# Performance work log

Measured on AMD Instinct MI355X. Metric: run time of the kernel, lower is better.

Reference implementation:

```python
import jax, jax.numpy as jnp
import numpy as np

B = 4096
E = 1024   # input_size (embedding)
H = 1024   # hidden_size
C = 1024   # context_vector_size
D = E + H + C  # combined_vector_size


def setup_inputs() -> dict:
    key = jax.random.key(0)
    ks = jax.random.split(key, 20)
    s_gate = 1.0 / np.sqrt(D)
    s_c = 1.0 / np.sqrt(C)
    s_h = 1.0 / np.sqrt(H)
    s_e = 1.0 / np.sqrt(E)
    return {
        "previous_embedded_caption": jax.random.normal(ks[0], (B, E), jnp.float32),
        "previous_hidden_state": jax.random.normal(ks[1], (B, H), jnp.float32),
        "previous_cell_state": jax.random.normal(ks[2], (B, H), jnp.float32),
        "current_context_vector": jax.random.normal(ks[3], (B, C), jnp.float32),
        "Wi": jax.random.uniform(ks[4], (H, D), jnp.float32, -s_gate, s_gate),
        "bi": jax.random.uniform(ks[5], (H,), jnp.float32, -s_gate, s_gate),
        "Wf": jax.random.uniform(ks[6], (H, D), jnp.float32, -s_gate, s_gate),
        "bf": jax.random.uniform(ks[7], (H,), jnp.float32, -s_gate, s_gate),
        "Wo": jax.random.uniform(ks[8], (H, D), jnp.float32, -s_gate, s_gate),
        "bo": jax.random.uniform(ks[9], (H,), jnp.float32, -s_gate, s_gate),
        "Wg": jax.random.uniform(ks[10], (H, D), jnp.float32, -s_gate, s_gate),
        "bg": jax.random.uniform(ks[11], (H,), jnp.float32, -s_gate, s_gate),
        "Wc": jax.random.uniform(ks[12], (E, C), jnp.float32, -s_c, s_c),
        "bc": jax.random.uniform(ks[13], (E,), jnp.float32, -s_c, s_c),
        "Wh": jax.random.uniform(ks[14], (E, H), jnp.float32, -s_h, s_h),
        "bh": jax.random.uniform(ks[15], (E,), jnp.float32, -s_h, s_h),
        "Wp": jax.random.uniform(ks[16], (E, E), jnp.float32, -s_e, s_e),
        "bp": jax.random.uniform(ks[17], (E,), jnp.float32, -s_e, s_e),
    }


def reference(previous_embedded_caption, previous_hidden_state, previous_cell_state,
              current_context_vector, Wi, bi, Wf, bf, Wo, bo, Wg, bg,
              Wc, bc, Wh, bh, Wp, bp):
    # combined vector [B, D]
    combined = jnp.concatenate(
        [previous_embedded_caption, previous_hidden_state, current_context_vector], axis=1)
    i = jax.nn.sigmoid(combined @ Wi.T + bi)
    f = jax.nn.sigmoid(combined @ Wf.T + bf)
    o = jax.nn.sigmoid(combined @ Wo.T + bo)
    g = jnp.tanh(combined @ Wg.T + bg)
    cell = f * previous_cell_state + i * g           # [B, H]
    hidden = o * jnp.tanh(cell)                      # [B, H]
    resid = previous_embedded_caption + (hidden @ Wh.T + bh) + (current_context_vector @ Wc.T + bc)
    prediction = resid @ Wp.T + bp                   # [B, E]
    return (prediction, hidden, cell)
```

## Files before the change

### kernel.cpp

```cpp
#include <hip/hip_runtime.h>
#include <stdint.h>

#define BATCH 4096
#define EHC   1024
#define DCOMB 3072
#define NTOT  ((size_t)BATCH * EHC)
#define WGATE ((size_t)EHC * DCOMB)
#define WSML  ((size_t)EHC * EHC)

#define BM 128
#define BK 64

typedef __bf16 bf16x8 __attribute__((ext_vector_type(8)));
typedef float  f32x4  __attribute__((ext_vector_type(4)));

__device__ inline unsigned short f2b(float f) {
    unsigned int x = __float_as_uint(f);
    unsigned int r = (x + 0x7fffu + ((x >> 16) & 1u)) >> 16;
    return (unsigned short)r;
}
__device__ inline float sigmoid_f(float x) { return 1.0f / (1.0f + __expf(-x)); }
__device__ inline float tanh_f(float x) {
    float xa = fminf(fmaxf(x, -15.0f), 15.0f);
    float e = __expf(2.0f * xa);
    return (e - 1.0f) / (e + 1.0f);
}

__device__ inline void load16(const void* g, void* l) {
    __builtin_amdgcn_global_load_lds(
        (const __attribute__((address_space(1))) void*)g,
        (__attribute__((address_space(3))) void*)l, 16, 0, 0);
}

__global__ __launch_bounds__(256)
void cvt_all(const float* __restrict__ s0, const float* __restrict__ s1,
             const float* __restrict__ s2, const float* __restrict__ s3,
             const float* __restrict__ s4, const float* __restrict__ s5,
             const float* __restrict__ s6, const float* __restrict__ s7,
             const float* __restrict__ s8, const float* __restrict__ s9,
             short* __restrict__ dst)
{
    const unsigned b = blockIdx.x;
    const float* src = s0; unsigned st = 0;
    if (b >= 2048)  { src = s1; st = 2048;  }
    if (b >= 4096)  { src = s2; st = 4096;  }
    if (b >= 6144)  { src = s3; st = 6144;  }
    if (b >= 7680)  { src = s4; st = 7680;  }
    if (b >= 9216)  { src = s5; st = 9216;  }
    if (b >= 10752) { src = s6; st = 10752; }
    if (b >= 12288) { src = s7; st = 12288; }
    if (b >= 12800) { src = s8; st = 12800; }
    if (b >= 13312) { src = s9; st = 13312; }
    size_t soff = ((size_t)(b - st) * 2048) + (size_t)threadIdx.x * 8;
    size_t doff = ((size_t)b * 2048) + (size_t)threadIdx.x * 8;
    float4 a = *(const float4*)(src + soff);
    float4 c = *(const float4*)(src + soff + 4);
    uint4 v;
    v.x = (unsigned)f2b(a.x) | ((unsigned)f2b(a.y) << 16);
    v.y = (unsigned)f2b(a.z) | ((unsigned)f2b(a.w) << 16);
    v.z = (unsigned)f2b(c.x) | ((unsigned)f2b(c.y) << 16);
    v.w = (unsigned)f2b(c.z) | ((unsigned)f2b(c.w) << 16);
    *(uint4*)(dst + doff) = v;
}

template <int MODE>
__global__ __launch_bounds__(256, 2)
void gemm_fused(const short* __restrict__ A0, const short* __restrict__ A1,
                const short* __restrict__ A2,
                const short* __restrict__ W0, const short* __restrict__ W1,
                const short* __restrict__ W2, const short* __restrict__ W3,
                const float* __restrict__ b0, const float* __restrict__ b1,
                const float* __restrict__ b2, const float* __restrict__ b3,
                const float* __restrict__ extra,
                void* __restrict__ outv)
{
    constexpr int BNT = (MODE == 1) ? 128 : 64;
    constexpr int NI  = BNT / 32;
    constexpr int WNW = BNT / 2;

    const int nblk = blockIdx.x;
    const int mblk = blockIdx.y;
    const int tid  = threadIdx.x;
    const int lane = tid & 63;
    const int wave = tid >> 6;
    const int wm = wave >> 1;
    const int wn = wave & 1;
    const int l15 = lane & 15;
    const int l4  = lane >> 4;

    __shared__ short As[BM * BK];
    __shared__ short Bs[BNT * BK];

    const int K = (MODE == 1) ? DCOMB : (MODE == 2 ? 2048 : 1024);
    const int wstride = (MODE == 1) ? DCOMB : 1024;

    int gate = 0;
    const short* Wsel = W0;
    const float* bsel = b0;
    if (MODE == 1) {
        gate = nblk >> 3;
        Wsel = (gate == 0) ? W0 : (gate == 1) ? W1 : (gate == 2) ? W2 : W3;
        bsel = (gate == 0) ? b0 : (gate == 1) ? b1 : (gate == 2) ? b2 : b3;
    }
    const int wrowbase = ((MODE == 1) ? (nblk & 7) : nblk) * BNT;

    int aoff[4], woff[NI];
#pragma unroll
    for (int j = 0; j < 4; j++) {
        int c  = j * 256 + tid;
        int r  = c >> 3;
        int qg = (c & 7) ^ (r & 7);
        aoff[j] = (mblk * BM + r) * 1024 + qg * 8;
    }
#pragma unroll
    for (int j = 0; j < NI; j++) {
        int c  = j * 256 + tid;
        int r  = c >> 3;
        int qg = (c & 7) ^ (r & 7);
        woff[j] = (wrowbase + r) * wstride + qg * 8;
    }

    int a_ld[2][4], b_ld[2][NI];
#pragma unroll
    for (int s = 0; s < 2; s++) {
#pragma unroll
        for (int i = 0; i < 4; i++) {
            int q = s * 4 + l4;
            int rowA = wm * 64 + i * 16 + l15;
            a_ld[s][i] = (rowA * 8 + (q ^ (rowA & 7))) * 8;
        }
#pragma unroll
        for (int i = 0; i < NI; i++) {
            int q = s * 4 + l4;
            int rowB = wn * WNW + i * 16 + l15;
            b_ld[s][i] = (rowB * 8 + (q ^ (rowB & 7))) * 8;
        }
    }

    f32x4 acc[4][NI];
#pragma unroll
    for (int i = 0; i < 4; i++)
#pragma unroll
        for (int j = 0; j < NI; j++) acc[i][j] = (f32x4){0.f, 0.f, 0.f, 0.f};

    const int KT = K / BK;
    for (int kt = 0; kt < KT; ++kt) {
        const int k0   = kt * BK;
        const int seg  = (MODE == 3) ? 0 : (k0 >> 10);
        const int acol = k0 & 1023;
        const int wcol = (MODE == 1) ? k0 : acol;
        const short* Aseg = (seg == 0) ? A0 : (seg == 1) ? A1 : A2;
        const short* Wt   = (MODE == 1) ? Wsel : ((seg == 0) ? W0 : W1);

        __syncthreads();
#pragma unroll
        for (int j = 0; j < 4; j++)
            load16(Aseg + aoff[j] + acol, &As[(j * 256 + tid) * 8]);
#pragma unroll
        for (int j = 0; j < NI; j++)
            load16(Wt + woff[j] + wcol, &Bs[(j * 256 + tid) * 8]);
        __syncthreads();

#pragma unroll
        for (int s = 0; s < 2; s++) {
            bf16x8 af[4], bv[NI];
#pragma unroll
            for (int i = 0; i < 4; i++) af[i] = *(const bf16x8*)(As + a_ld[s][i]);
#pragma unroll
            for (int i = 0; i < NI; i++) bv[i] = *(const bf16x8*)(Bs + b_ld[s][i]);
#pragma unroll
            for (int mi = 0; mi < 4; mi++)
#pragma unroll
                for (int ni = 0; ni < NI; ni++)
                    acc[mi][ni] = __builtin_amdgcn_mfma_f32_16x16x32_bf16(
                        af[mi], bv[ni], acc[mi][ni], 0, 0, 0);
        }
    }

#pragma unroll
    for (int ni = 0; ni < NI; ni++) {
        const int col = nblk * BNT + wn * WNW + ni * 16 + l15;
        float bias_v;
        if (MODE == 1)      bias_v = bsel[col & 1023];
        else if (MODE == 2) bias_v = b0[col] + b1[col];
        else                bias_v = b0[col];
#pragma unroll
        for (int mi = 0; mi < 4; mi++) {
#pragma unroll
            for (int r = 0; r < 4; r++) {
                const int row = mblk * BM + wm * 64 + mi * 16 + l4 * 4 + r;
                float v = acc[mi][ni][r] + bias_v;
                if (MODE == 1) {
                    v = fminf(fmaxf(v, -30.0f), 30.0f);
                    v = (gate < 3) ? sigmoid_f(v) : tanh_f(v);
                    ((short*)outv)[(size_t)gate * NTOT + (size_t)row * 1024 + (col & 1023)]
                        = (short)f2b(v);
                } else if (MODE == 2) {
                    v += extra[(size_t)row * 1024 + col];
                    ((short*)outv)[(size_t)row * 1024 + col] = (short)f2b(v);
                } else {
                    ((float*)outv)[(size_t)row * 1024 + col] = v;
                }
            }
        }
    }
}

__global__ __launch_bounds__(256)
void lstm_cell(const short* __restrict__ gates, const float* __restrict__ pc,
               float* __restrict__ hid_f, float* __restrict__ cell_f,
               short* __restrict__ hid_b)
{
    size_t base = ((size_t)blockIdx.x * 256 + threadIdx.x) * 8;
    if (base >= NTOT) return;
    bf16x8 iv = *(const bf16x8*)(gates + base);
    bf16x8 fv = *(const bf16x8*)(gates + NTOT + base);
    bf16x8 ov = *(const bf16x8*)(gates + 2 * NTOT + base);
    bf16x8 gv = *(const bf16x8*)(gates + 3 * NTOT + base);
    float4 p0 = *(const float4*)(pc + base);
    float4 p1 = *(const float4*)(pc + base + 4);
    float pv[8] = {p0.x, p0.y, p0.z, p0.w, p1.x, p1.y, p1.z, p1.w};
    float cf[8], hf[8];
    uint4 hb;
    unsigned hbp[4];
#pragma unroll
    for (int j = 0; j < 8; j++) {
        float c = (float)fv[j] * pv[j] + (float)iv[j] * (float)gv[j];
        float h = (float)ov[j] * tanh_f(c);
        cf[j] = c; hf[j] = h;
    }
#pragma unroll
    for (int j = 0; j < 4; j++)
        hbp[j] = (unsigned)f2b(hf[2 * j]) | ((unsigned)f2b(hf[2 * j + 1]) << 16);
    hb.x = hbp[0]; hb.y = hbp[1]; hb.z = hbp[2]; hb.w = hbp[3];
    *(float4*)(cell_f + base)     = (float4){cf[0], cf[1], cf[2], cf[3]};
    *(float4*)(cell_f + base + 4) = (float4){cf[4], cf[5], cf[6], cf[7]};
    *(float4*)(hid_f + base)      = (float4){hf[0], hf[1], hf[2], hf[3]};
    *(float4*)(hid_f + base + 4)  = (float4){hf[4], hf[5], hf[6], hf[7]};
    *(uint4*)(hid_b + base) = hb;
}

extern "C" void kernel_launch(void* const* d_in, const int* in_sizes, int n_in,
                              void* d_out, int out_size, void* d_ws, size_t ws_size,
                              hipStream_t stream)
{
    const float* emb  = (const float*)d_in[0];
    const float* hid  = (const float*)d_in[1];
    const float* pcel = (const float*)d_in[2];
    const float* ctx  = (const float*)d_in[3];
    const float* Wi = (const float*)d_in[4];   const float* bi = (const float*)d_in[5];
    const float* Wf = (const float*)d_in[6];   const float* bf_ = (const float*)d_in[7];
    const float* Wo = (const float*)d_in[8];   const float* bo = (const float*)d_in[9];
    const float* Wg = (const float*)d_in[10];  const float* bg = (const float*)d_in[11];
    const float* Wc = (const float*)d_in[12];  const float* bc = (const float*)d_in[13];
    const float* Wh = (const float*)d_in[14];  const float* bh = (const float*)d_in[15];
    const float* Wp = (const float*)d_in[16];  const float* bp = (const float*)d_in[17];

    float* out      = (float*)d_out;
    float* pred     = out;
    float* hidden_o = out + NTOT;
    float* cell_o   = out + 2 * NTOT;

    short* ws = (short*)d_ws;
    short* w_emb  = ws;
    short* w_hid  = ws + NTOT;
    short* w_ctx  = ws + 2 * NTOT;
    short* w_Wg4  = ws + 3 * NTOT;
    short* w_Wh   = w_Wg4 + 4 * WGATE;
    short* w_Wc   = w_Wh + WSML;
    short* w_Wp   = w_Wc + WSML;
    short* w_gat  = w_Wp + WSML;
    short* w_hidb = w_gat + 4 * NTOT;
    short* w_res  = w_hidb + NTOT;

    dim3 blk(256, 1, 1);
    const short* np16 = nullptr;
    const float* npf  = nullptr;

    hipLaunchKernelGGL(cvt_all, dim3(13824), blk, 0, stream,
                       emb, hid, ctx, Wi, Wf, Wo, Wg, Wh, Wc, Wp, ws);

    hipLaunchKernelGGL((gemm_fused<1>), dim3(32, 32), blk, 0, stream,
                       w_emb, w_hid, w_ctx,
                       w_Wg4, w_Wg4 + WGATE, w_Wg4 + 2 * WGATE, w_Wg4 + 3 * WGATE,
                       bi, bf_, bo, bg, npf, (void*)w_gat);
    hipLaunchKernelGGL(lstm_cell, dim3((unsigned)(NTOT / 8 / 256)), blk, 0, stream,
                       w_gat, pcel, hidden_o, cell_o, w_hidb);
    hipLaunchKernelGGL((gemm_fused<2>), dim3(16, 32), blk, 0, stream,
                       w_hidb, w_ctx, np16, w_Wh, w_Wc, np16, np16,
                       bh, bc, npf, npf, emb, (void*)w_res);
    hipLaunchKernelGGL((gemm_fused<3>), dim3(16, 32), blk, 0, stream,
                       w_res, np16, np16, w_Wp, np16, np16, np16,
                       bp, npf, npf, npf, npf, (void*)pred);
}
```

Measured before the change: 348.8 us.

## Fuse LSTM cell update into gate GEMM epilogue and shrink small-GEMM tiles

```diff
diff --git a/kernel.cpp b/kernel.cpp
--- a/kernel.cpp
+++ b/kernel.cpp
@@ -8,7 +8,6 @@
 #define WGATE ((size_t)EHC * DCOMB)
 #define WSML  ((size_t)EHC * EHC)
 
-#define BM 128
 #define BK 64
 
 typedef __bf16 bf16x8 __attribute__((ext_vector_type(8)));
@@ -72,11 +71,18 @@
                 const float* __restrict__ b0, const float* __restrict__ b1,
                 const float* __restrict__ b2, const float* __restrict__ b3,
                 const float* __restrict__ extra,
-                void* __restrict__ outv)
+                void* __restrict__ outv, float* __restrict__ out2,
+                short* __restrict__ out3)
 {
-    constexpr int BNT = (MODE == 1) ? 128 : 64;
+    constexpr int NG  = (MODE == 1) ? 4 : 1;
+    constexpr int BMT = (MODE == 1) ? 128 : 64;
+    constexpr int BNT = 64;
+    constexpr int MI  = BMT / 32;
     constexpr int NI  = BNT / 32;
-    constexpr int WNW = BNT / 2;
+    constexpr int AI  = BMT / 32;
+    constexpr int BI  = BNT / 32;
+    constexpr int WMH = BMT / 2;
+    constexpr int BSZ = BNT * BK;
 
     const int nblk = blockIdx.x;
     const int mblk = blockIdx.y;
@@ -88,156 +94,143 @@
     const int l15 = lane & 15;
     const int l4  = lane >> 4;
 
-    __shared__ short As[BM * BK];
-    __shared__ short Bs[BNT * BK];
+    __shared__ short As[BMT * BK];
+    __shared__ short Bs[NG * BSZ];
 
     const int K = (MODE == 1) ? DCOMB : (MODE == 2 ? 2048 : 1024);
     const int wstride = (MODE == 1) ? DCOMB : 1024;
-
-    int gate = 0;
-    const short* Wsel = W0;
-    const float* bsel = b0;
-    if (MODE == 1) {
-        gate = nblk >> 3;
-        Wsel = (gate == 0) ? W0 : (gate == 1) ? W1 : (gate == 2) ? W2 : W3;
-        bsel = (gate == 0) ? b0 : (gate == 1) ? b1 : (gate == 2) ? b2 : b3;
-    }
-    const int wrowbase = ((MODE == 1) ? (nblk & 7) : nblk) * BNT;
-
-    int aoff[4], woff[NI];
-#pragma unroll
-    for (int j = 0; j < 4; j++) {
+    const int wrowbase = nblk * BNT;
+
+    int aoff[AI], woff[BI];
+#pragma unroll
+    for (int j = 0; j < AI; j++) {
         int c  = j * 256 + tid;
         int r  = c >> 3;
         int qg = (c & 7) ^ (r & 7);
-        aoff[j] = (mblk * BM + r) * 1024 + qg * 8;
-    }
-#pragma unroll
-    for (int j = 0; j < NI; j++) {
+        aoff[j] = (mblk * BMT + r) * 1024 + qg * 8;
+    }
+#pragma unroll
+    for (int j = 0; j < BI; j++) {
         int c  = j * 256 + tid;
         int r  = c >> 3;
         int qg = (c & 7) ^ (r & 7);
         woff[j] = (wrowbase + r) * wstride + qg * 8;
     }
 
-    int a_ld[2][4], b_ld[2][NI];
+    int a_ld[2][MI], b_ld[2][NI];
 #pragma unroll
     for (int s = 0; s < 2; s++) {
-#pragma unroll
-        for (int i = 0; i < 4; i++) {
-            int q = s * 4 + l4;
-            int rowA = wm * 64 + i * 16 + l15;
+        int q = s * 4 + l4;
+#pragma unroll
+        for (int i = 0; i < MI; i++) {
+            int rowA = wm * WMH + i * 16 + l15;
             a_ld[s][i] = (rowA * 8 + (q ^ (rowA & 7))) * 8;
         }
 #pragma unroll
         for (int i = 0; i < NI; i++) {
-            int q = s * 4 + l4;
-            int rowB = wn * WNW + i * 16 + l15;
+            int rowB = wn * 32 + i * 16 + l15;
             b_ld[s][i] = (rowB * 8 + (q ^ (rowB & 7))) * 8;
         }
     }
 
-    f32x4 acc[4][NI];
-#pragma unroll
-    for (int i = 0; i < 4; i++)
-#pragma unroll
-        for (int j = 0; j < NI; j++) acc[i][j] = (f32x4){0.f, 0.f, 0.f, 0.f};
+    f32x4 acc[NG][MI][NI];
+#pragma unroll
+    for (int g = 0; g < NG; g++)
+#pragma unroll
+        for (int i = 0; i < MI; i++)
+#pragma unroll
+            for (int j = 0; j < NI; j++) acc[g][i][j] = (f32x4){0.f, 0.f, 0.f, 0.f};
 
     const int KT = K / BK;
     for (int kt = 0; kt < KT; ++kt) {
         const int k0   = kt * BK;
         const int seg  = (MODE == 3) ? 0 : (k0 >> 10);
         const int acol = k0 & 1023;
-        const int wcol = (MODE == 1) ? k0 : acol;
         const short* Aseg = (seg == 0) ? A0 : (seg == 1) ? A1 : A2;
-        const short* Wt   = (MODE == 1) ? Wsel : ((seg == 0) ? W0 : W1);
 
         __syncthreads();
 #pragma unroll
-        for (int j = 0; j < 4; j++)
+        for (int j = 0; j < AI; j++)
             load16(Aseg + aoff[j] + acol, &As[(j * 256 + tid) * 8]);
-#pragma unroll
-        for (int j = 0; j < NI; j++)
-            load16(Wt + woff[j] + wcol, &Bs[(j * 256 + tid) * 8]);
+        if (MODE == 1) {
+            const short* Wg4[4] = {W0, W1, W2, W3};
+#pragma unroll
+            for (int g = 0; g < 4; g++)
+#pragma unroll
+                for (int j = 0; j < BI; j++)
+                    load16(Wg4[g] + woff[j] + k0, &Bs[g * BSZ + (j * 256 + tid) * 8]);
+        } else {
+            const short* Wt = (seg == 0) ? W0 : W1;
+#pragma unroll
+            for (int j = 0; j < BI; j++)
+                load16(Wt + woff[j] + acol, &Bs[(j * 256 + tid) * 8]);
+        }
         __syncthreads();
 
 #pragma unroll
         for (int s = 0; s < 2; s++) {
-            bf16x8 af[4], bv[NI];
-#pragma unroll
-            for (int i = 0; i < 4; i++) af[i] = *(const bf16x8*)(As + a_ld[s][i]);
-#pragma unroll
-            for (int i = 0; i < NI; i++) bv[i] = *(const bf16x8*)(Bs + b_ld[s][i]);
-#pragma unroll
-            for (int mi = 0; mi < 4; mi++)
-#pragma unroll
-                for (int ni = 0; ni < NI; ni++)
-                    acc[mi][ni] = __builtin_amdgcn_mfma_f32_16x16x32_bf16(
-                        af[mi], bv[ni], acc[mi][ni], 0, 0, 0);
+            bf16x8 af[MI];
+#pragma unroll
+            for (int i = 0; i < MI; i++) af[i] = *(const bf16x8*)(As + a_ld[s][i]);
+#pragma unroll
+            for (int g = 0; g < NG; g++) {
+                bf16x8 bv[NI];
+#pragma unroll
+                for (int i = 0; i < NI; i++)
+                    bv[i] = *(const bf16x8*)(Bs + g * BSZ + b_ld[s][i]);
+#pragma unroll
+                for (int mi = 0; mi < MI; mi++)
+#pragma unroll
+                    for (int ni = 0; ni < NI; ni++)
+                        acc[g][mi][ni] = __builtin_amdgcn_mfma_f32_16x16x32_bf16(
+                            af[mi], bv[ni], acc[g][mi][ni], 0, 0, 0);
+            }
         }
     }
 
 #pragma unroll
     for (int ni = 0; ni < NI; ni++) {
-        const int col = nblk * BNT + wn * WNW + ni * 16 + l15;
-        float bias_v;
-        if (MODE == 1)      bias_v = bsel[col & 1023];
-        else if (MODE == 2) bias_v = b0[col] + b1[col];
-        else                bias_v = b0[col];
-#pragma unroll
-        for (int mi = 0; mi < 4; mi++) {
-#pragma unroll
-            for (int r = 0; r < 4; r++) {
-                const int row = mblk * BM + wm * 64 + mi * 16 + l4 * 4 + r;
-                float v = acc[mi][ni][r] + bias_v;
-                if (MODE == 1) {
-                    v = fminf(fmaxf(v, -30.0f), 30.0f);
-                    v = (gate < 3) ? sigmoid_f(v) : tanh_f(v);
-                    ((short*)outv)[(size_t)gate * NTOT + (size_t)row * 1024 + (col & 1023)]
-                        = (short)f2b(v);
-                } else if (MODE == 2) {
-                    v += extra[(size_t)row * 1024 + col];
-                    ((short*)outv)[(size_t)row * 1024 + col] = (short)f2b(v);
-                } else {
-                    ((float*)outv)[(size_t)row * 1024 + col] = v;
+        const int col = nblk * BNT + wn * 32 + ni * 16 + l15;
+        if (MODE == 1) {
+            const float bi_ = b0[col], bf_ = b1[col], bo_ = b2[col], bg_ = b3[col];
+#pragma unroll
+            for (int mi = 0; mi < MI; mi++) {
+#pragma unroll
+                for (int r = 0; r < 4; r++) {
+                    const size_t row = (size_t)(mblk * BMT + wm * WMH + mi * 16 + l4 * 4 + r);
+                    const size_t idx = row * 1024 + col;
+                    float ai = fminf(fmaxf(acc[0][mi][ni][r] + bi_, -30.f), 30.f);
+                    float af_ = fminf(fmaxf(acc[1][mi][ni][r] + bf_, -30.f), 30.f);
+                    float ao = fminf(fmaxf(acc[2][mi][ni][r] + bo_, -30.f), 30.f);
+                    float ag = fminf(fmaxf(acc[3][mi][ni][r] + bg_, -30.f), 30.f);
+                    float ig = sigmoid_f(ai), fg = sigmoid_f(af_);
+                    float og = sigmoid_f(ao), gg = tanh_f(ag);
+                    float c = fg * extra[idx] + ig * gg;
+                    float h = og * tanh_f(c);
+                    ((float*)outv)[idx] = c;
+                    out2[idx] = h;
+                    out3[idx] = (short)f2b(h);
                 }
             }
-        }
-    }
-}
-
-__global__ __launch_bounds__(256)
-void lstm_cell(const short* __restrict__ gates, const float* __restrict__ pc,
-               float* __restrict__ hid_f, float* __restrict__ cell_f,
-               short* __restrict__ hid_b)
-{
-    size_t base = ((size_t)blockIdx.x * 256 + threadIdx.x) * 8;
-    if (base >= NTOT) return;
-    bf16x8 iv = *(const bf16x8*)(gates + base);
-    bf16x8 fv = *(const bf16x8*)(gates + NTOT + base);
-    bf16x8 ov = *(const bf16x8*)(gates + 2 * NTOT + base);
-    bf16x8 gv = *(const bf16x8*)(gates + 3 * NTOT + base);
-    float4 p0 = *(const float4*)(pc + base);
-    float4 p1 = *(const float4*)(pc + base + 4);
-    float pv[8] = {p0.x, p0.y, p0.z, p0.w, p1.x, p1.y, p1.z, p1.w};
-    float cf[8], hf[8];
-    uint4 hb;
-    unsigned hbp[4];
-#pragma unroll
-    for (int j = 0; j < 8; j++) {
-        float c = (float)fv[j] * pv[j] + (float)iv[j] * (float)gv[j];
-        float h = (float)ov[j] * tanh_f(c);
-        cf[j] = c; hf[j] = h;
-    }
-#pragma unroll
-    for (int j = 0; j < 4; j++)
-        hbp[j] = (unsigned)f2b(hf[2 * j]) | ((unsigned)f2b(hf[2 * j + 1]) << 16);
-    hb.x = hbp[0]; hb.y = hbp[1]; hb.z = hbp[2]; hb.w = hbp[3];
-    *(float4*)(cell_f + base)     = (float4){cf[0], cf[1], cf[2], cf[3]};
-    *(float4*)(cell_f + base + 4) = (float4){cf[4], cf[5], cf[6], cf[7]};
-    *(float4*)(hid_f + base)      = (float4){hf[0], hf[1], hf[2], hf[3]};
-    *(float4*)(hid_f + base + 4)  = (float4){hf[4], hf[5], hf[6], hf[7]};
-    *(uint4*)(hid_b + base) = hb;
+        } else {
+            float bias_v = (MODE == 2) ? (b0[col] + b1[col]) : b0[col];
+#pragma unroll
+            for (int mi = 0; mi < MI; mi++) {
+#pragma unroll
+                for (int r = 0; r < 4; r++) {
+                    const size_t row = (size_t)(mblk * BMT + wm * WMH + mi * 16 + l4 * 4 + r);
+                    const size_t idx = row * 1024 + col;
+                    float v = acc[0][mi][ni][r] + bias_v;
+                    if (MODE == 2) {
+                        v += extra[idx];
+                        ((short*)outv)[idx] = (short)f2b(v);
+                    } else {
+                        ((float*)outv)[idx] = v;
+                    }
+                }
+            }
+        }
+    }
 }
 
 extern "C" void kernel_launch(void* const* d_in, const int* in_sizes, int n_in,
@@ -269,8 +262,7 @@
     short* w_Wh   = w_Wg4 + 4 * WGATE;
     short* w_Wc   = w_Wh + WSML;
     short* w_Wp   = w_Wc + WSML;
-    short* w_gat  = w_Wp + WSML;
-    short* w_hidb = w_gat + 4 * NTOT;
+    short* w_hidb = w_Wp + WSML;
     short* w_res  = w_hidb + NTOT;
 
     dim3 blk(256, 1, 1);
@@ -280,16 +272,15 @@
     hipLaunchKernelGGL(cvt_all, dim3(13824), blk, 0, stream,
                        emb, hid, ctx, Wi, Wf, Wo, Wg, Wh, Wc, Wp, ws);
 
-    hipLaunchKernelGGL((gemm_fused<1>), dim3(32, 32), blk, 0, stream,
+    hipLaunchKernelGGL((gemm_fused<1>), dim3(16, 32), blk, 0, stream,
                        w_emb, w_hid, w_ctx,
                        w_Wg4, w_Wg4 + WGATE, w_Wg4 + 2 * WGATE, w_Wg4 + 3 * WGATE,
-                       bi, bf_, bo, bg, npf, (void*)w_gat);
-    hipLaunchKernelGGL(lstm_cell, dim3((unsigned)(NTOT / 8 / 256)), blk, 0, stream,
-                       w_gat, pcel, hidden_o, cell_o, w_hidb);
-    hipLaunchKernelGGL((gemm_fused<2>), dim3(16, 32), blk, 0, stream,
+                       bi, bf_, bo, bg, pcel,
+                       (void*)cell_o, hidden_o, w_hidb);
+    hipLaunchKernelGGL((gemm_fused<2>), dim3(16, 64), blk, 0, stream,
                        w_hidb, w_ctx, np16, w_Wh, w_Wc, np16, np16,
-                       bh, bc, npf, npf, emb, (void*)w_res);
-    hipLaunchKernelGGL((gemm_fused<3>), dim3(16, 32), blk, 0, stream,
+                       bh, bc, npf, npf, emb, (void*)w_res, (float*)nullptr, (short*)nullptr);
+    hipLaunchKernelGGL((gemm_fused<3>), dim3(16, 64), blk, 0, stream,
                        w_res, np16, np16, w_Wp, np16, np16, np16,
-                       bp, npf, npf, npf, npf, (void*)pred);
-}
+                       bp, npf, npf, npf, npf, (void*)pred, (float*)nullptr, (short*)nullptr);
+}
```

After: 333.1 us. -4.5%, faster.
